# Kernel tuning notes

Measured on AMD Instinct MI355X. Metric: run time of the kernel, lower is better.

## Reference

```python
import jax, jax.numpy as jnp
import numpy as np

N = 8192        # points
M = 131072      # query-key pairs (edges)
C_IN = 512
H = 8           # heads
D = 64          # head_channels
BINS = 48
BIN_SIZE = 0.05


def setup_inputs() -> dict:
    key = jax.random.key(0)
    ks = jax.random.split(key, 8)
    x_F = jax.random.normal(ks[0], (N, C_IN), dtype=jnp.float32)
    x_C = jax.random.uniform(ks[1], (N, 3), dtype=jnp.float32)
    qk_pair_idxs = jax.random.randint(ks[2], (2, M), 0, N, dtype=jnp.int64)
    W_qkv = jax.random.normal(ks[3], (C_IN, 3 * H * D), dtype=jnp.float32) * 0.02
    b_qkv = jnp.zeros((3 * H * D,), dtype=jnp.float32)
    q_tables = jax.random.normal(ks[4], (3, BINS, H, D), dtype=jnp.float32) * 0.02
    k_tables = jax.random.normal(ks[5], (3, BINS, H, D), dtype=jnp.float32) * 0.02
    v_tables = jax.random.normal(ks[6], (3, BINS, H, D), dtype=jnp.float32) * 0.02
    return {"x_F": x_F, "x_C": x_C, "qk_pair_idxs": qk_pair_idxs,
            "W_qkv": W_qkv, "b_qkv": b_qkv,
            "q_tables": q_tables, "k_tables": k_tables, "v_tables": v_tables}


def reference(x_F, x_C, qk_pair_idxs, W_qkv, b_qkv, q_tables, k_tables, v_tables):
    n = x_F.shape[0]
    qkv = (x_F @ W_qkv + b_qkv).reshape(n, 3, H, D)
    q = qkv[:, 0] * (D ** -0.5)   # scale folded into queries, as in the module
    k = qkv[:, 1]
    v = qkv[:, 2]
    qi = qk_pair_idxs[0]
    ki = qk_pair_idxs[1]
    # quantized relative coordinates -> table bin indices [M,3]
    rel = (x_C[qi] - x_C[ki]) / BIN_SIZE + BINS / 2
    idx = jnp.clip(rel.astype(jnp.int32), 0, BINS - 1)
    # precompute per-point, per-axis, per-bin table dot products [N,3,BINS,H]
    q_dot = jnp.einsum('nhd,abhd->nabh', q, q_tables)
    k_dot = jnp.einsum('nhd,abhd->nabh', k, k_tables)
    # content logits [M,H]
    logits = jnp.einsum('mhd,mhd->mh', q[qi], k[ki])
    for a in range(3):  # fixed xyz axes
        logits = logits + q_dot[qi, a, idx[:, a]] + k_dot[ki, a, idx[:, a]]
    # scatter softmax over query index (per head)
    seg_max = jax.ops.segment_max(logits, qi, num_segments=n)
    e = jnp.exp(logits - seg_max[qi])
    denom = jax.ops.segment_sum(e, qi, num_segments=n)
    attn = e / denom[qi]  # [M,H]
    # value-side relative position bias, summed over axes [M,H,D]
    vt = v_tables[0, idx[:, 0]] + v_tables[1, idx[:, 1]] + v_tables[2, idx[:, 2]]
    contrib = attn[:, :, None] * (v[ki] + vt)            # [M,H,D]
    agg = jax.ops.segment_sum(contrib, qi, num_segments=n)  # [N,H,D]
    return agg.reshape(n, H * D)
```

## Files before the change

kernel.cpp:

```cpp
#include <hip/hip_runtime.h>
#include <hip/hip_bf16.h>
#include <stdint.h>

#define N_PTS 8192
#define M_EDGES 131072
#define CIN 512
#define QKV_COLS 1536

typedef __bf16 bf16x8 __attribute__((ext_vector_type(8)));
typedef float f32x4 __attribute__((ext_vector_type(4)));

#define GAS __attribute__((address_space(1)))
#define LAS __attribute__((address_space(3)))

__device__ __forceinline__ void gload_lds16(const void* g, void* l) {
  __builtin_amdgcn_global_load_lds((const GAS void*)g, (LAS void*)l, 16, 0, 0);
}

__global__ __launch_bounds__(256) void prep_kernel(
    const float* __restrict__ xF, const float* __restrict__ W,
    const float* __restrict__ qt, const float* __restrict__ kt,
    const float* __restrict__ vt, const int* __restrict__ pairs,
    const float* __restrict__ xc,
    __bf16* __restrict__ A, __bf16* __restrict__ BT,
    __bf16* __restrict__ qtb, __bf16* __restrict__ ktb, __bf16* __restrict__ vtT,
    int* __restrict__ qi_a, unsigned* __restrict__ pack0, int* __restrict__ cnt) {
  __shared__ float tile[32][33];
  int b = blockIdx.x;
  int tid = threadIdx.x;
  if (b < 4096) {
    int base = (b * 256 + tid) * 4;
    float4 v = *(const float4*)(xF + base);
    A[base + 0] = (__bf16)v.x;
    A[base + 1] = (__bf16)v.y;
    A[base + 2] = (__bf16)v.z;
    A[base + 3] = (__bf16)v.w;
  } else if (b < 4864) {
    int blk = b - 4096;
    int bk = blk & 15, bn = blk >> 4;
    int x = tid & 31, y = tid >> 5;
#pragma unroll
    for (int j = 0; j < 4; j++) {
      int r = y + j * 8;
      tile[r][x] = W[(size_t)(bk * 32 + r) * QKV_COLS + bn * 32 + x];
    }
    __syncthreads();
#pragma unroll
    for (int j = 0; j < 4; j++) {
      int r = y + j * 8;
      BT[(size_t)(bn * 32 + r) * CIN + bk * 32 + x] = (__bf16)tile[x][r];
    }
  } else if (b < 5152) {
    int i = (b - 4864) * 256 + tid;
    int d = i & 63, h = (i >> 6) & 7, ab = i >> 9;
    int po = (h * 144 + ab) * 64 + d;
    qtb[po] = (__bf16)qt[i];
    ktb[po] = (__bf16)kt[i];
  } else if (b < 5472) {
    int i = (b - 5152) * 256 + tid;
    int p = i % 160;
    int d = (i / 160) & 63;
    int h = i / 10240;
    vtT[i] = (p < 144) ? (__bf16)vt[p * 512 + h * 64 + d] : (__bf16)0.f;
  } else {
    int m = (b - 5472) * 256 + tid;
    int qi = pairs[m], ki = pairs[M_EDGES + m];
    unsigned pb = 0;
#pragma unroll
    for (int a = 0; a < 3; a++) {
      float rel = (xc[qi * 3 + a] - xc[ki * 3 + a]) / 0.05f + 24.0f;
      int bb = (int)rel;
      bb = bb < 0 ? 0 : (bb > 47 ? 47 : bb);
      pb |= (unsigned)bb << (6 * a);
    }
    qi_a[m] = qi;
    pack0[m] = (unsigned)ki | (pb << 13);
    atomicAdd(&cnt[qi], 1);
  }
}

__global__ __launch_bounds__(256) void gemm_qkv(const __bf16* __restrict__ A,
                                                const __bf16* __restrict__ BT,
                                                const float* __restrict__ bias,
                                                __bf16* __restrict__ qb,
                                                __bf16* __restrict__ kb,
                                                __bf16* __restrict__ vb) {
  __shared__ __align__(16) char At[2][64 * 128];
  __shared__ __align__(16) char Bt[2][128 * 128];
  int tid = threadIdx.x;
  int w = tid >> 6, l = tid & 63;
  int bn = blockIdx.x, bm = blockIdx.y;
  int wm = w & 1, wn = w >> 1;
  f32x4 acc[2][4] = {};
  const char* Ab = (const char*)A;
  const char* Bb = (const char*)BT;
  int lr = l & 15;
  int lk = (l >> 4) * 16;
  int xr = (lr & 7) << 4;

  auto stage = [&](int tk, int buf) {
#pragma unroll
    for (int r = 0; r < 2; r++) {
      int flat = r * 4096 + tid * 16;
      int row = flat >> 7, colb = flat & 127;
      int gcolb = colb ^ ((row & 7) << 4);
      gload_lds16(Ab + ((size_t)(bm * 64 + row) * CIN + tk * 64) * 2 + gcolb,
                  At[buf] + r * 4096 + w * 1024);
    }
#pragma unroll
    for (int r = 0; r < 4; r++) {
      int flat = r * 4096 + tid * 16;
      int row = flat >> 7, colb = flat & 127;
      int gcolb = colb ^ ((row & 7) << 4);
      gload_lds16(Bb + ((size_t)(bn * 128 + row) * CIN + tk * 64) * 2 + gcolb,
                  Bt[buf] + r * 4096 + w * 1024);
    }
  };

  stage(0, 0);
  __syncthreads();
  int cur = 0;
  for (int kt = 0; kt < 8; kt++) {
    if (kt < 7) stage(kt + 1, cur ^ 1);
#pragma unroll
    for (int ks = 0; ks < 2; ks++) {
      bf16x8 af[2], bfr[4];
      int cs = (ks * 64 + lk) ^ xr;
#pragma unroll
      for (int mf = 0; mf < 2; mf++) af[mf] = *(const bf16x8*)(At[cur] + (wm * 32 + mf * 16 + lr) * 128 + cs);
#pragma unroll
      for (int nf = 0; nf < 4; nf++) bfr[nf] = *(const bf16x8*)(Bt[cur] + (wn * 64 + nf * 16 + lr) * 128 + cs);
#pragma unroll
      for (int mf = 0; mf < 2; mf++)
#pragma unroll
        for (int nf = 0; nf < 4; nf++)
          acc[mf][nf] = __builtin_amdgcn_mfma_f32_16x16x32_bf16(af[mf], bfr[nf], acc[mf][nf], 0, 0, 0);
    }
    __syncthreads();
    cur ^= 1;
  }

  int lg = l >> 4;
#pragma unroll
  for (int mf = 0; mf < 2; mf++) {
#pragma unroll
    for (int nf = 0; nf < 4; nf++) {
      int gc = bn * 128 + wn * 64 + nf * 16 + lr;
      float b = bias[gc];
      int which = gc >> 9;
      int col = gc & 511;
      __bf16* dst = which == 0 ? qb : (which == 1 ? kb : vb);
      float scale = which == 0 ? 0.125f : 1.0f;
#pragma unroll
      for (int j = 0; j < 4; j++) {
        int gr = bm * 64 + wm * 32 + mf * 16 + lg * 4 + j;
        dst[(size_t)gr * 512 + col] = (__bf16)((acc[mf][nf][j] + b) * scale);
      }
    }
  }
}

__global__ __launch_bounds__(256) void table_dot(const __bf16* __restrict__ qb,
                                                 const __bf16* __restrict__ kb,
                                                 const __bf16* __restrict__ qtb,
                                                 const __bf16* __restrict__ ktb,
                                                 __bf16* __restrict__ qdot,
                                                 __bf16* __restrict__ kdot) {
  __shared__ __align__(16) char As[128 * 128];
  __shared__ __align__(16) char Bs[144 * 128];
  int nt = blockIdx.x, h = blockIdx.y, z = blockIdx.z;
  const __bf16* src = z ? kb : qb;
  const __bf16* tab = z ? ktb : qtb;
  __bf16* out = z ? kdot : qdot;
  int tid = threadIdx.x, w = tid >> 6, l = tid & 63;
  const char* sb = (const char*)src;
  const char* tb = (const char*)tab + (size_t)h * 144 * 128;
#pragma unroll
  for (int p = 0; p < 4; p++) {
    int flat = p * 4096 + tid * 16;
    int row = flat >> 7, colb = flat & 127;
    int gcolb = colb ^ ((row & 7) << 4);
    gload_lds16(sb + (size_t)(nt * 128 + row) * 1024 + h * 128 + gcolb, As + p * 4096 + w * 1024);
    gload_lds16(tb + row * 128 + gcolb, Bs + p * 4096 + w * 1024);
  }
  if (w < 2) {
    int flat = 16384 + w * 1024 + l * 16;
    int row = flat >> 7, colb = flat & 127;
    int gcolb = colb ^ ((row & 7) << 4);
    gload_lds16(tb + row * 128 + gcolb, Bs + 16384 + w * 1024);
  }
  __syncthreads();

  f32x4 acc[2][9] = {};
  int lr = l & 15, lk = (l >> 4) * 16;
  int xr = (lr & 7) << 4;
#pragma unroll
  for (int ks = 0; ks < 2; ks++) {
    bf16x8 af[2], bf[9];
    int cs = (ks * 64 + lk) ^ xr;
#pragma unroll
    for (int mf = 0; mf < 2; mf++)
      af[mf] = *(const bf16x8*)(As + (w * 32 + mf * 16 + lr) * 128 + cs);
#pragma unroll
    for (int nf = 0; nf < 9; nf++)
      bf[nf] = *(const bf16x8*)(Bs + (nf * 16 + lr) * 128 + cs);
#pragma unroll
    for (int mf = 0; mf < 2; mf++)
#pragma unroll
      for (int nf = 0; nf < 9; nf++)
        acc[mf][nf] = __builtin_amdgcn_mfma_f32_16x16x32_bf16(af[mf], bf[nf], acc[mf][nf], 0, 0, 0);
  }

  int lg = l >> 4;
#pragma unroll
  for (int mf = 0; mf < 2; mf++)
#pragma unroll
    for (int nf = 0; nf < 9; nf++)
#pragma unroll
      for (int j = 0; j < 4; j++) {
        int n = nt * 128 + w * 32 + mf * 16 + lg * 4 + j;
        int ab = nf * 16 + lr;
        out[(size_t)n * 1152 + ab * 8 + h] = (__bf16)acc[mf][nf][j];
      }
}

__global__ __launch_bounds__(256) void scan_kernel(const int* __restrict__ cnt,
                                                   int* __restrict__ off,
                                                   int* __restrict__ cursor) {
  __shared__ int wsum[4];
  int tid = threadIdx.x, lane = tid & 63, w = tid >> 6;
  int local[32];
  int s = 0;
#pragma unroll
  for (int i = 0; i < 8; i++) {
    int4 v = ((const int4*)cnt)[tid * 8 + i];
    local[i * 4 + 0] = v.x; local[i * 4 + 1] = v.y;
    local[i * 4 + 2] = v.z; local[i * 4 + 3] = v.w;
    s += v.x + v.y + v.z + v.w;
  }
  int incl = s;
#pragma unroll
  for (int d = 1; d < 64; d <<= 1) {
    int t = __shfl_up(incl, d, 64);
    if (lane >= d) incl += t;
  }
  if (lane == 63) wsum[w] = incl;
  __syncthreads();
  int woff = 0;
#pragma unroll
  for (int j = 0; j < 4; j++) woff += (j < w) ? wsum[j] : 0;
  int run = woff + incl - s;
  int base = tid * 32;
#pragma unroll
  for (int i = 0; i < 32; i++) {
    off[base + i] = run;
    cursor[base + i] = run;
    run += local[i];
  }
  if (tid == 255) off[N_PTS] = run;
}

__global__ void scatter_k(const int* __restrict__ qi_a, const unsigned* __restrict__ pack0,
                          int* __restrict__ cursor, unsigned* __restrict__ epack) {
  int m = blockIdx.x * blockDim.x + threadIdx.x;
  if (m < M_EDGES) {
    int qi = qi_a[m];
    int pos = atomicAdd(&cursor[qi], 1);
    epack[pos] = pack0[m];
  }
}

__global__ __launch_bounds__(512) void attn_kernel(
    const __bf16* __restrict__ qb, const __bf16* __restrict__ kb,
    const __bf16* __restrict__ vb, const __bf16* __restrict__ qdot,
    const __bf16* __restrict__ kdot, const int* __restrict__ off,
    const unsigned* __restrict__ epack,
    float* __restrict__ num, float* __restrict__ den, __bf16* __restrict__ Hb) {
  __shared__ float hist[8 * 164];
  __shared__ float part[8][512];
  __shared__ float dpart[8][8];
  int n = blockIdx.x;
  int tid = threadIdx.x;
  int w = tid >> 6, l = tid & 63;
  int h = l >> 3, dg = l & 7;

  for (int i = tid; i < 8 * 164; i += 512) hist[i] = 0.f;
  __syncthreads();

  bf16x8 q8 = *(const bf16x8*)(qb + (n << 9) + l * 8);
  float qv[8];
#pragma unroll
  for (int j = 0; j < 8; j++) qv[j] = (float)q8[j];

  float acc[8] = {0.f, 0.f, 0.f, 0.f, 0.f, 0.f, 0.f, 0.f};
  float dn = 0.f;
  int e0 = off[n], e1 = off[n + 1];
  const __bf16* qd_row = qdot + (size_t)n * 1152;
  int axis = dg < 3 ? dg : dg - 3;
  int tsh = 6 * axis;

  for (int e = e0 + w; e < e1; e += 8) {
    unsigned pk = epack[__builtin_amdgcn_readfirstlane(e)];
    int ki = pk & 8191;
    unsigned pb = pk >> 13;
    bf16x8 k8 = *(const bf16x8*)(kb + (ki << 9) + l * 8);
    bf16x8 v8 = *(const bf16x8*)(vb + (ki << 9) + l * 8);
    int bin = (int)((pb >> tsh) & 63u);
    int idx = (axis * 48 + bin) * 8 + h;
    const __bf16* tbl = dg < 3 ? qd_row : (kdot + (size_t)ki * 1152);
    float p = (dg < 6) ? (float)tbl[idx] : 0.f;
#pragma unroll
    for (int j = 0; j < 8; j++) p += qv[j] * (float)k8[j];
    p += __shfl_xor(p, 1, 64);
    p += __shfl_xor(p, 2, 64);
    p += __shfl_xor(p, 4, 64);
    float x = __expf(p);
    dn += x;
#pragma unroll
    for (int j = 0; j < 8; j++) acc[j] += x * (float)v8[j];
    if (dg == 0) {
      float* hh = hist + h * 164;
      atomicAdd(hh + (pb & 63), x);
      atomicAdd(hh + 48 + ((pb >> 6) & 63), x);
      atomicAdd(hh + 96 + ((pb >> 12) & 63), x);
    }
  }

  f32x4 a0 = {acc[0], acc[1], acc[2], acc[3]};
  f32x4 a1 = {acc[4], acc[5], acc[6], acc[7]};
  *(f32x4*)&part[w][l * 8] = a0;
  *(f32x4*)&part[w][l * 8 + 4] = a1;
  if (dg == 0) dpart[w][h] = dn;
  __syncthreads();

  float s = 0.f;
#pragma unroll
  for (int ww = 0; ww < 8; ww++) s += part[ww][tid];
  num[(n << 9) + tid] = s;
  if (tid < 8) {
    float d = 0.f;
#pragma unroll
    for (int ww = 0; ww < 8; ww++) d += dpart[ww][tid];
    den[n * 8 + tid] = d;
  }
  for (int i = tid; i < 1280; i += 512) {
    int hh = i / 160, p = i % 160;
    Hb[(size_t)n * 1280 + i] = (__bf16)hist[hh * 164 + p];
  }
}

__global__ __launch_bounds__(256) void finish_kernel(const __bf16* __restrict__ Hb,
                                                     const __bf16* __restrict__ vtT,
                                                     const float* __restrict__ den,
                                                     float* __restrict__ out) {
  __shared__ __align__(16) char As[2][128 * 64];
  __shared__ __align__(16) char Bs[2][64 * 64];
  int nt = blockIdx.x, h = blockIdx.y;
  int tid = threadIdx.x, w = tid >> 6, l = tid & 63;
  int lr = l & 15, lk = (l >> 4) * 16;
  int xr = (lr & 3) << 4;
  const char* Ab = (const char*)Hb;
  const char* Bb = (const char*)vtT;
  f32x4 acc[2][4] = {};

  auto stage = [&](int tk, int buf) {
#pragma unroll
    for (int c = 0; c < 2; c++) {
      int flat = c * 4096 + tid * 16;
      int row = flat >> 6, colb = flat & 63;
      int gcolb = colb ^ ((row & 3) << 4);
      gload_lds16(Ab + ((size_t)(nt * 128 + row) * 1280 + h * 160 + tk * 32) * 2 + gcolb,
                  As[buf] + c * 4096 + w * 1024);
    }
    {
      int flat = tid * 16;
      int row = flat >> 6, colb = flat & 63;
      int gcolb = colb ^ ((row & 3) << 4);
      gload_lds16(Bb + ((size_t)(h * 64 + row) * 160 + tk * 32) * 2 + gcolb,
                  Bs[buf] + w * 1024);
    }
  };

  stage(0, 0);
  __syncthreads();
  int cur = 0;
  for (int kt = 0; kt < 5; kt++) {
    if (kt < 4) stage(kt + 1, cur ^ 1);
    bf16x8 af[2], bf[4];
    int cs = lk ^ xr;
#pragma unroll
    for (int mf = 0; mf < 2; mf++) af[mf] = *(const bf16x8*)(As[cur] + (w * 32 + mf * 16 + lr) * 64 + cs);
#pragma unroll
    for (int nf = 0; nf < 4; nf++) bf[nf] = *(const bf16x8*)(Bs[cur] + (nf * 16 + lr) * 64 + cs);
#pragma unroll
    for (int mf = 0; mf < 2; mf++)
#pragma unroll
      for (int nf = 0; nf < 4; nf++)
        acc[mf][nf] = __builtin_amdgcn_mfma_f32_16x16x32_bf16(af[mf], bf[nf], acc[mf][nf], 0, 0, 0);
    __syncthreads();
    cur ^= 1;
  }

  int lg = l >> 4;
#pragma unroll
  for (int mf = 0; mf < 2; mf++) {
#pragma unroll
    for (int j = 0; j < 4; j++) {
      int n = nt * 128 + w * 32 + mf * 16 + lg * 4 + j;
      float dnv = den[n * 8 + h];
      float inv = dnv > 0.f ? 1.f / dnv : 0.f;
#pragma unroll
      for (int nf = 0; nf < 4; nf++) {
        int gi = (n << 9) + h * 64 + nf * 16 + lr;
        out[gi] = (out[gi] + acc[mf][nf][j]) * inv;
      }
    }
  }
}

extern "C" void kernel_launch(void* const* d_in, const int* in_sizes, int n_in,
                              void* d_out, int out_size, void* d_ws, size_t ws_size,
                              hipStream_t stream) {
  const float* xF = (const float*)d_in[0];
  const float* xC = (const float*)d_in[1];
  const int* pairs = (const int*)d_in[2];
  const float* W = (const float*)d_in[3];
  const float* bias = (const float*)d_in[4];
  const float* qt = (const float*)d_in[5];
  const float* kt = (const float*)d_in[6];
  const float* vt = (const float*)d_in[7];
  float* out = (float*)d_out;

  char* ws = (char*)d_ws;
  size_t o = 0;
  auto alloc = [&](size_t bytes) {
    void* p = ws + o;
    o = (o + bytes + 255) & ~(size_t)255;
    return p;
  };
  char* region0 = (char*)alloc((size_t)N_PTS * 1280 * 2);
  __bf16* A = (__bf16*)region0;
  __bf16* BT = (__bf16*)(region0 + (size_t)N_PTS * CIN * 2);
  __bf16* Hb = (__bf16*)region0;
  __bf16* qb = (__bf16*)alloc((size_t)N_PTS * 512 * 2);
  __bf16* kb = (__bf16*)alloc((size_t)N_PTS * 512 * 2);
  __bf16* vb = (__bf16*)alloc((size_t)N_PTS * 512 * 2);
  __bf16* qtb = (__bf16*)alloc((size_t)8 * 144 * 64 * 2);
  __bf16* ktb = (__bf16*)alloc((size_t)8 * 144 * 64 * 2);
  __bf16* vtT = (__bf16*)alloc((size_t)8 * 64 * 160 * 2);
  __bf16* qdot = (__bf16*)alloc((size_t)N_PTS * 1152 * 2);
  __bf16* kdot = (__bf16*)alloc((size_t)N_PTS * 1152 * 2);
  float* den = (float*)alloc((size_t)N_PTS * 8 * 4);
  int* qi_a = (int*)alloc(M_EDGES * 4);
  unsigned* pack0 = (unsigned*)alloc(M_EDGES * 4);
  unsigned* epack = (unsigned*)alloc(M_EDGES * 4);
  int* cnt = (int*)alloc(N_PTS * 4);
  int* off = (int*)alloc((N_PTS + 1) * 4);
  int* cursor = (int*)alloc(N_PTS * 4);

  hipMemsetAsync(cnt, 0, N_PTS * 4, stream);

  prep_kernel<<<5984, 256, 0, stream>>>(xF, W, qt, kt, vt, pairs, xC,
                                        A, BT, qtb, ktb, vtT, qi_a, pack0, cnt);
  scan_kernel<<<1, 256, 0, stream>>>(cnt, off, cursor);
  scatter_k<<<M_EDGES / 256, 256, 0, stream>>>(qi_a, pack0, cursor, epack);
  gemm_qkv<<<dim3(QKV_COLS / 128, N_PTS / 64), 256, 0, stream>>>(A, BT, bias, qb, kb, vb);
  table_dot<<<dim3(N_PTS / 128, 8, 2), 256, 0, stream>>>(qb, kb, qtb, ktb, qdot, kdot);
  attn_kernel<<<N_PTS, 512, 0, stream>>>(qb, kb, vb, qdot, kdot, off, epack, out, den, Hb);
  finish_kernel<<<dim3(N_PTS / 128, 8), 256, 0, stream>>>(Hb, vtT, den, out);
}
```

Baseline: 156.8 us.

## Fold scan into GEMM launch and precompute per-edge key bias in scatter

The single-block prefix scan becomes an extra block of the QKV GEMM launch, removing one kernel launch. The scatter kernel now runs after table_dot and, for each edge, gathers the three key-side table-dot rows, sums them and writes a per-edge 8-head bias (khat) in CSR order. The attention kernel then reads one contiguous bias value per head instead of three scattered kdot reads, so fewer lanes take part in bias gathering. The cost is an extra M x 8 bf16 buffer and a scatter that now does gathers, and the bias is rounded to bf16 after being summed.

```diff
diff --git a/kernel.cpp b/kernel.cpp
--- a/kernel.cpp
+++ b/kernel.cpp
@@ -79,17 +79,53 @@
   }
 }
 
-__global__ __launch_bounds__(256) void gemm_qkv(const __bf16* __restrict__ A,
-                                                const __bf16* __restrict__ BT,
-                                                const float* __restrict__ bias,
-                                                __bf16* __restrict__ qb,
-                                                __bf16* __restrict__ kb,
-                                                __bf16* __restrict__ vb) {
+__global__ __launch_bounds__(256) void gemm_scan_kernel(
+    const __bf16* __restrict__ A, const __bf16* __restrict__ BT,
+    const float* __restrict__ bias, __bf16* __restrict__ qb,
+    __bf16* __restrict__ kb, __bf16* __restrict__ vb,
+    const int* __restrict__ cnt, int* __restrict__ off, int* __restrict__ cursor) {
   __shared__ __align__(16) char At[2][64 * 128];
   __shared__ __align__(16) char Bt[2][128 * 128];
+  __shared__ int wsum[4];
+  int bid = blockIdx.x;
   int tid = threadIdx.x;
+
+  if (bid == 1536) {
+    int lane = tid & 63, w = tid >> 6;
+    int local[32];
+    int s = 0;
+#pragma unroll
+    for (int i = 0; i < 8; i++) {
+      int4 v = ((const int4*)cnt)[tid * 8 + i];
+      local[i * 4 + 0] = v.x; local[i * 4 + 1] = v.y;
+      local[i * 4 + 2] = v.z; local[i * 4 + 3] = v.w;
+      s += v.x + v.y + v.z + v.w;
+    }
+    int incl = s;
+#pragma unroll
+    for (int d = 1; d < 64; d <<= 1) {
+      int t = __shfl_up(incl, d, 64);
+      if (lane >= d) incl += t;
+    }
+    if (lane == 63) wsum[w] = incl;
+    __syncthreads();
+    int woff = 0;
+#pragma unroll
+    for (int j = 0; j < 4; j++) woff += (j < w) ? wsum[j] : 0;
+    int run = woff + incl - s;
+    int base = tid * 32;
+#pragma unroll
+    for (int i = 0; i < 32; i++) {
+      off[base + i] = run;
+      cursor[base + i] = run;
+      run += local[i];
+    }
+    if (tid == 255) off[N_PTS] = run;
+    return;
+  }
+
+  int bn = bid % 12, bm = bid / 12;
   int w = tid >> 6, l = tid & 63;
-  int bn = blockIdx.x, bm = blockIdx.y;
   int wm = w & 1, wn = w >> 1;
   f32x4 acc[2][4] = {};
   const char* Ab = (const char*)A;
@@ -224,56 +260,32 @@
       }
 }
 
-__global__ __launch_bounds__(256) void scan_kernel(const int* __restrict__ cnt,
-                                                   int* __restrict__ off,
-                                                   int* __restrict__ cursor) {
-  __shared__ int wsum[4];
-  int tid = threadIdx.x, lane = tid & 63, w = tid >> 6;
-  int local[32];
-  int s = 0;
-#pragma unroll
-  for (int i = 0; i < 8; i++) {
-    int4 v = ((const int4*)cnt)[tid * 8 + i];
-    local[i * 4 + 0] = v.x; local[i * 4 + 1] = v.y;
-    local[i * 4 + 2] = v.z; local[i * 4 + 3] = v.w;
-    s += v.x + v.y + v.z + v.w;
-  }
-  int incl = s;
-#pragma unroll
-  for (int d = 1; d < 64; d <<= 1) {
-    int t = __shfl_up(incl, d, 64);
-    if (lane >= d) incl += t;
-  }
-  if (lane == 63) wsum[w] = incl;
-  __syncthreads();
-  int woff = 0;
-#pragma unroll
-  for (int j = 0; j < 4; j++) woff += (j < w) ? wsum[j] : 0;
-  int run = woff + incl - s;
-  int base = tid * 32;
-#pragma unroll
-  for (int i = 0; i < 32; i++) {
-    off[base + i] = run;
-    cursor[base + i] = run;
-    run += local[i];
-  }
-  if (tid == 255) off[N_PTS] = run;
-}
-
 __global__ void scatter_k(const int* __restrict__ qi_a, const unsigned* __restrict__ pack0,
-                          int* __restrict__ cursor, unsigned* __restrict__ epack) {
+                          const __bf16* __restrict__ kdot, int* __restrict__ cursor,
+                          unsigned* __restrict__ epack, __bf16* __restrict__ khat) {
   int m = blockIdx.x * blockDim.x + threadIdx.x;
-  if (m < M_EDGES) {
-    int qi = qi_a[m];
-    int pos = atomicAdd(&cursor[qi], 1);
-    epack[pos] = pack0[m];
-  }
+  if (m >= M_EDGES) return;
+  int qi = qi_a[m];
+  unsigned pk = pack0[m];
+  int pos = atomicAdd(&cursor[qi], 1);
+  epack[pos] = pk;
+  int ki = pk & 8191;
+  unsigned pb = pk >> 13;
+  const __bf16* kd = kdot + (size_t)ki * 1152;
+  bf16x8 t0 = *(const bf16x8*)(kd + ((pb & 63u)) * 8);
+  bf16x8 t1 = *(const bf16x8*)(kd + (48 + ((pb >> 6) & 63u)) * 8);
+  bf16x8 t2 = *(const bf16x8*)(kd + (96 + ((pb >> 12) & 63u)) * 8);
+  bf16x8 o;
+#pragma unroll
+  for (int j = 0; j < 8; j++)
+    o[j] = (__bf16)((float)t0[j] + (float)t1[j] + (float)t2[j]);
+  *(bf16x8*)(khat + ((size_t)pos << 3)) = o;
 }
 
 __global__ __launch_bounds__(512) void attn_kernel(
     const __bf16* __restrict__ qb, const __bf16* __restrict__ kb,
     const __bf16* __restrict__ vb, const __bf16* __restrict__ qdot,
-    const __bf16* __restrict__ kdot, const int* __restrict__ off,
+    const __bf16* __restrict__ khat, const int* __restrict__ off,
     const unsigned* __restrict__ epack,
     float* __restrict__ num, float* __restrict__ den, __bf16* __restrict__ Hb) {
   __shared__ float hist[8 * 164];
@@ -296,8 +308,6 @@
   float dn = 0.f;
   int e0 = off[n], e1 = off[n + 1];
   const __bf16* qd_row = qdot + (size_t)n * 1152;
-  int axis = dg < 3 ? dg : dg - 3;
-  int tsh = 6 * axis;
 
   for (int e = e0 + w; e < e1; e += 8) {
     unsigned pk = epack[__builtin_amdgcn_readfirstlane(e)];
@@ -305,10 +315,15 @@
     unsigned pb = pk >> 13;
     bf16x8 k8 = *(const bf16x8*)(kb + (ki << 9) + l * 8);
     bf16x8 v8 = *(const bf16x8*)(vb + (ki << 9) + l * 8);
-    int bin = (int)((pb >> tsh) & 63u);
-    int idx = (axis * 48 + bin) * 8 + h;
-    const __bf16* tbl = dg < 3 ? qd_row : (kdot + (size_t)ki * 1152);
-    float p = (dg < 6) ? (float)tbl[idx] : 0.f;
+    float p;
+    if (dg < 3) {
+      int bin = (int)((pb >> (6 * dg)) & 63u);
+      p = (float)qd_row[(dg * 48 + bin) * 8 + h];
+    } else if (dg == 3) {
+      p = (float)khat[((size_t)e << 3) + h];
+    } else {
+      p = 0.f;
+    }
 #pragma unroll
     for (int j = 0; j < 8; j++) p += qv[j] * (float)k8[j];
     p += __shfl_xor(p, 1, 64);
@@ -450,6 +465,7 @@
   __bf16* vtT = (__bf16*)alloc((size_t)8 * 64 * 160 * 2);
   __bf16* qdot = (__bf16*)alloc((size_t)N_PTS * 1152 * 2);
   __bf16* kdot = (__bf16*)alloc((size_t)N_PTS * 1152 * 2);
+  __bf16* khat = (__bf16*)alloc((size_t)M_EDGES * 8 * 2);
   float* den = (float*)alloc((size_t)N_PTS * 8 * 4);
   int* qi_a = (int*)alloc(M_EDGES * 4);
   unsigned* pack0 = (unsigned*)alloc(M_EDGES * 4);
@@ -462,10 +478,9 @@
 
   prep_kernel<<<5984, 256, 0, stream>>>(xF, W, qt, kt, vt, pairs, xC,
                                         A, BT, qtb, ktb, vtT, qi_a, pack0, cnt);
-  scan_kernel<<<1, 256, 0, stream>>>(cnt, off, cursor);
-  scatter_k<<<M_EDGES / 256, 256, 0, stream>>>(qi_a, pack0, cursor, epack);
-  gemm_qkv<<<dim3(QKV_COLS / 128, N_PTS / 64), 256, 0, stream>>>(A, BT, bias, qb, kb, vb);
+  gemm_scan_kernel<<<1537, 256, 0, stream>>>(A, BT, bias, qb, kb, vb, cnt, off, cursor);
   table_dot<<<dim3(N_PTS / 128, 8, 2), 256, 0, stream>>>(qb, kb, qtb, ktb, qdot, kdot);
-  attn_kernel<<<N_PTS, 512, 0, stream>>>(qb, kb, vb, qdot, kdot, off, epack, out, den, Hb);
+  scatter_k<<<M_EDGES / 256, 256, 0, stream>>>(qi_a, pack0, kdot, cursor, epack, khat);
+  attn_kernel<<<N_PTS, 512, 0, stream>>>(qb, kb, vb, qdot, khat, off, epack, out, den, Hb);
   finish_kernel<<<dim3(N_PTS / 128, 8), 256, 0, stream>>>(Hb, vtT, den, out);
 }
```

Result: no change. 157.8 us (+0.6%).
